# Kernel optimization log

Hardware: AMD Instinct MI355X
Metric: run time of the kernel (lower is better)

The kernel has to match this reference:

```python
import jax, jax.numpy as jnp
import numpy as np

P, N, C, F = 3, 50000, 5, 68   # planes, nodes/plane, classes, in+node feats
E = 150000                     # edges/plane
EF, NF = 64, 64                # edge_features, node_features

def setup_inputs() -> dict:
    key = jax.random.key(0)
    ks = jax.random.split(key, 10)
    s = 0.1
    return {
        "x": jax.random.normal(ks[0], (P, N, C, F), jnp.float32),
        "edge_index": jax.random.randint(ks[1], (P, 2, E), 0, N, jnp.int64),
        "ew1": s * jax.random.normal(ks[2], (P, C, 2 * F, EF), jnp.float32),
        "eb1": s * jax.random.normal(ks[3], (P, C, EF), jnp.float32),
        "ew2": s * jax.random.normal(ks[4], (P, C, EF, 1), jnp.float32),
        "eb2": s * jax.random.normal(ks[5], (P, C, 1), jnp.float32),
        "nw1": s * jax.random.normal(ks[6], (P, C, 2 * F, NF), jnp.float32),
        "nb1": s * jax.random.normal(ks[7], (P, C, NF), jnp.float32),
        "nw2": s * jax.random.normal(ks[8], (P, C, NF, NF), jnp.float32),
        "nb2": s * jax.random.normal(ks[9], (P, C, NF), jnp.float32),
    }

def _plane(x, ei, ew1, eb1, ew2, eb2, nw1, nb1, nw2, nb2):
    # x: [N, C, F]; ei: [2, E]
    src, dst = ei[0], ei[1]
    x_j = x[src]                                   # [E, C, F] (source)
    x_i = x[dst]                                   # [E, C, F] (target)
    # edge net input is detached in the original module
    e_in = jax.lax.stop_gradient(jnp.concatenate([x_i, x_j], axis=-1))  # [E, C, 2F]
    h = jnp.tanh(jnp.einsum('ecf,cfo->eco', e_in, ew1) + eb1)           # [E, C, EF]
    logit = jnp.einsum('ecf,cfo->eco', h, ew2) + eb2                    # [E, C, 1]
    w = jax.nn.softmax(logit, axis=1)              # softmax over classes
    msg = w * x_j                                  # [E, C, F]
    aggr = jax.ops.segment_sum(msg, dst, num_segments=x.shape[0])       # [N, C, F]
    u_in = jnp.concatenate([x, aggr], axis=-1)     # [N, C, 2F]
    h2 = jnp.tanh(jnp.einsum('ncf,cfo->nco', u_in, nw1) + nb1)          # [N, C, NF]
    return jnp.tanh(jnp.einsum('ncf,cfo->nco', h2, nw2) + nb2)          # [N, C, NF]

def reference(x, edge_index, ew1, eb1, ew2, eb2, nw1, nb1, nw2, nb2):
    return jax.vmap(_plane)(x, edge_index, ew1, eb1, ew2, eb2, nw1, nb1, nw2, nb2)
```

## Files before the change

### kernel.cpp

```cpp
#include <hip/hip_runtime.h>
#include <hip/hip_fp16.h>
#include <math.h>

typedef unsigned int uint;
typedef __fp16 half2_t __attribute__((ext_vector_type(2)));
typedef _Float16 v8h __attribute__((ext_vector_type(8)));
typedef _Float16 v4h __attribute__((ext_vector_type(4)));
typedef float f32v4 __attribute__((ext_vector_type(4)));

#define NUM_P 3
#define NUM_N 50000
#define NUM_C 5
#define NUM_E 150000
#define CF 340
#define NB32 1563
#define TE 128
#define EB2 1172
#define TN 128
#define NB128 391
#define SROW 129
#define NSB 196
#define NSBP 50176

#define AH_T   ((size_t)NUM_P * NUM_N * 170)
#define NW1_T  (NUM_P * NUM_C * 68 * 64)
#define NW2_T  (NUM_P * NUM_C * 32 * 64)
#define LG_T   ((size_t)NUM_P * NUM_C * NUM_E)
#define EWB_T  (NUM_P * NUM_C * 2 * 4 * 640)

__device__ __forceinline__ float fast_tanh(float x) {
    float a = __expf(2.0f * x);
    float t = __builtin_amdgcn_rcpf(a + 1.0f);
    return fmaf(-2.0f, t, 1.0f);
}

__device__ __forceinline__ float dot2f(half2_t a, half2_t b, float c) {
#if __has_builtin(__builtin_amdgcn_fdot2)
    return __builtin_amdgcn_fdot2(a, b, c, false);
#else
    return fmaf((float)a[0], (float)b[0], fmaf((float)a[1], (float)b[1], c));
#endif
}

__device__ __forceinline__ half2_t bc(uint u) { return __builtin_bit_cast(half2_t, u); }

__device__ __forceinline__ uint pk2(float a, float b) {
    half2_t h = __builtin_amdgcn_cvt_pkrtz(a, b);
    return __builtin_bit_cast(uint, h);
}

__device__ __forceinline__ v8h mk8(uint a, uint b, uint c, uint d) {
    uint4 u; u.x = a; u.y = b; u.z = c; u.w = d;
    return __builtin_bit_cast(v8h, u);
}

__global__ __launch_bounds__(256) void convert_x_kernel(
    const float4* __restrict__ x4, uint* __restrict__ xh,
    uint* __restrict__ xn, int write_xn)
{
    __shared__ uint lds[32 * 170];
    const int nb = blockIdx.x % NB32;
    const int p  = blockIdx.x / NB32;
    const int n0 = nb * 32;
    const int nvalid = (n0 + 32 <= NUM_N) ? 32 : (NUM_N - n0);
    const int t = threadIdx.x;

    const float4* src = x4 + ((size_t)p * NUM_N + n0) * 85;
    const int nf4 = nvalid * 85;
    #pragma unroll
    for (int it = 0; it < 11; ++it) {
        const int i = t + it * 256;
        if (i < nf4) {
            const float4 v = src[i];
            lds[2 * i]     = pk2(v.x, v.y);
            lds[2 * i + 1] = pk2(v.z, v.w);
        }
    }
    __syncthreads();

    const int nq = nvalid * 34;
    #pragma unroll 1
    for (int c = 0; c < NUM_C; ++c) {
        uint* dst = xh + ((size_t)(p * NUM_C + c) * NUM_N + n0) * 34;
        #pragma unroll
        for (int it = 0; it < 5; ++it) {
            const int i = t + it * 256;
            if (i < nq) {
                const int nl = i / 34, j = i - nl * 34;
                dst[i] = lds[nl * 170 + c * 34 + j];
            }
        }
    }

    if (write_xn) {
        uint* dstn = xn + ((size_t)p * NUM_N + n0) * 170;
        const int tot = nvalid * 170;
        #pragma unroll
        for (int it = 0; it < 22; ++it) {
            const int i = t + it * 256;
            if (i < tot) dstn[i] = lds[i];
        }
    }
}

__global__ __launch_bounds__(256) void pack_pairs_kernel(
    const float* __restrict__ in, uint* __restrict__ outp, int total)
{
    int i = blockIdx.x * 256 + threadIdx.x;
    if (i >= total) return;
    int t = i >> 6, o = i & 63;
    outp[i] = pk2(in[t * 128 + o], in[t * 128 + 64 + o]);
}

__global__ __launch_bounds__(256) void pack_edge_mfma_kernel(
    const float* __restrict__ ew1, uint* __restrict__ ewb)
{
    int i = blockIdx.x * 256 + threadIdx.x;
    if (i >= EWB_T) return;
    int g    = i / 5120;
    int rem  = i - g * 5120;
    int s    = rem / 2560;
    int rem2 = rem - s * 2560;
    int nt   = rem2 / 640;
    int u    = rem2 - nt * 640;

    int f0, o; bool valid;
    if (u < 512) {
        int kt = u >> 8, uu = u & 255;
        int lane = uu >> 2, pp = uu & 3;
        f0 = kt * 32 + (lane >> 4) * 8 + 2 * pp;
        o  = nt * 16 + (lane & 15);
        valid = true;
    } else {
        int uu = u - 512;
        int lane = uu >> 1, pp = uu & 1;
        f0 = 64 + (lane >> 4) * 4 + 2 * pp;
        o  = nt * 16 + (lane & 15);
        valid = ((lane >> 4) == 0);
    }
    float w0 = 0.f, w1 = 0.f;
    if (valid) {
        int f = s * 68 + f0;
        w0 = ew1[((size_t)g * 136 + f) * 64 + o];
        w1 = ew1[((size_t)g * 136 + f + 1) * 64 + o];
    }
    ewb[i] = pk2(w0, w1);
}

__global__ __launch_bounds__(128) void edge_mfma_kernel(
    const uint*  __restrict__ xh,
    const int*   __restrict__ ei,
    const uint*  __restrict__ ewb,
    const float* __restrict__ eb1,
    const float* __restrict__ ew2,
    const float* __restrict__ eb2,
    float*       __restrict__ logits)
{
    __shared__ uint smem[TE * 40];
    __shared__ int  ids[2][TE];

    const int g    = blockIdx.x / EB2;
    const int blk  = blockIdx.x - g * EB2;
    const int p    = g / NUM_C;
    const int e0   = blk * TE;
    const int t    = threadIdx.x;
    const int lane = t & 63;
    const int wv   = t >> 6;
    const int col  = lane & 15;
    const int G    = lane >> 4;

    {
        const int e  = e0 + t;
        const int ec = (e < NUM_E) ? e : (NUM_E - 1);
        ids[0][t] = ei[(p * 2 + 0) * NUM_E + ec];
        ids[1][t] = ei[(p * 2 + 1) * NUM_E + ec];
    }
    {
        const uint2 z = make_uint2(0u, 0u);
        *(uint2*)&smem[t * 40 + 34] = z;
        *(uint2*)&smem[t * 40 + 36] = z;
        *(uint2*)&smem[t * 40 + 38] = z;
    }

    const uint* slice = xh + (size_t)g * NUM_N * 34;

    float b1v[4], w2v[4];
    #pragma unroll
    for (int nt = 0; nt < 4; ++nt) {
        b1v[nt] = eb1[g * 64 + nt * 16 + col];
        w2v[nt] = ew2[g * 64 + nt * 16 + col];
    }

    f32v4 acc[4][4];
    #pragma unroll
    for (int m = 0; m < 4; ++m)
        #pragma unroll
        for (int nt = 0; nt < 4; ++nt) {
            f32v4 a = {b1v[nt], b1v[nt], b1v[nt], b1v[nt]};
            acc[m][nt] = a;
        }
    __syncthreads();

    #pragma unroll 1
    for (int side = 0; side < 2; ++side) {
        const int* idr = ids[1 - side];
        #pragma unroll
        for (int k = 0; k < 17; ++k) {
            const int i2 = t + TE * k;
            const int e  = i2 / 17, j2 = i2 - e * 17;
            const uint2 v = *(const uint2*)(slice + (size_t)idr[e] * 34 + 2 * j2);
            *(uint2*)&smem[e * 40 + 2 * j2] = v;
        }
        __syncthreads();

        const uint* wb = ewb + (size_t)((g * 2 + side) * 4) * 640;
        v8h B0[4], B1[4]; v4h B2[4];
        #pragma unroll
        for (int nt = 0; nt < 4; ++nt) {
            const uint* fb = wb + nt * 640;
            B0[nt] = __builtin_bit_cast(v8h, *(const uint4*)(fb + lane * 4));
            B1[nt] = __builtin_bit_cast(v8h, *(const uint4*)(fb + 256 + lane * 4));
            B2[nt] = __builtin_bit_cast(v4h, *(const uint2*)(fb + 512 + lane * 2));
        }

        #pragma unroll
        for (int m = 0; m < 4; ++m) {
            const uint* rp = &smem[(wv * 64 + m * 16 + col) * 40];
            const v8h A0 = __builtin_bit_cast(v8h, *(const uint4*)(rp + G * 4));
            const v8h A1 = __builtin_bit_cast(v8h, *(const uint4*)(rp + 16 + G * 4));
            const v4h A2 = __builtin_bit_cast(v4h, *(const uint2*)(rp + 32 + G * 2));
            #pragma unroll
            for (int nt = 0; nt < 4; ++nt) {
                acc[m][nt] = __builtin_amdgcn_mfma_f32_16x16x32_f16(A0, B0[nt], acc[m][nt], 0, 0, 0);
                acc[m][nt] = __builtin_amdgcn_mfma_f32_16x16x32_f16(A1, B1[nt], acc[m][nt], 0, 0, 0);
                acc[m][nt] = __builtin_amdgcn_mfma_f32_16x16x16f16(A2, B2[nt], acc[m][nt], 0, 0, 0);
            }
        }
        __syncthreads();
    }

    float* elds = (float*)smem;
    #pragma unroll
    for (int m = 0; m < 4; ++m) {
        #pragma unroll
        for (int r = 0; r < 4; ++r) {
            float part = 0.f;
            #pragma unroll
            for (int nt = 0; nt < 4; ++nt)
                part = fmaf(w2v[nt], fast_tanh(acc[m][nt][r]), part);
            elds[(wv * 64 + m * 16 + G * 4 + r) * 20 + col] = part;
        }
    }
    const float4 s0 = *(const float4*)&elds[t * 20 + 0];
    const float4 s1 = *(const float4*)&elds[t * 20 + 4];
    const float4 s2 = *(const float4*)&elds[t * 20 + 8];
    const float4 s3 = *(const float4*)&elds[t * 20 + 12];
    float lg = ((s0.x + s0.y) + (s0.z + s0.w)) + ((s1.x + s1.y) + (s1.z + s1.w))
             + ((s2.x + s2.y) + (s2.z + s2.w)) + ((s3.x + s3.y) + (s3.z + s3.w))
             + eb2[g];
    if (e0 + t < NUM_E) logits[(size_t)g * NUM_E + e0 + t] = lg;
}

__global__ __launch_bounds__(256) void deg_kernel(
    const int* __restrict__ ei, int* __restrict__ deg)
{
    const int i = blockIdx.x * 256 + threadIdx.x;
    if (i >= NUM_P * NUM_E) return;
    const int p = i / NUM_E, e = i - p * NUM_E;
    const int dst = ei[(p * 2 + 1) * NUM_E + e];
    atomicAdd(&deg[p * NUM_N + dst], 1);
}

__global__ __launch_bounds__(256) void scan_block_kernel(
    const int* __restrict__ deg, int* __restrict__ intra, int* __restrict__ bsum)
{
    __shared__ int s[256];
    const int blk = blockIdx.x % NSB;
    const int p   = blockIdx.x / NSB;
    const int t   = threadIdx.x;
    const int n   = blk * 256 + t;
    const int d   = (n < NUM_N) ? deg[p * NUM_N + n] : 0;
    s[t] = d;
    __syncthreads();
    #pragma unroll
    for (int o = 1; o < 256; o <<= 1) {
        int v = (t >= o) ? s[t - o] : 0;
        __syncthreads();
        s[t] += v;
        __syncthreads();
    }
    if (n < NUM_N) intra[p * NSBP + n] = s[t] - d;
    if (t == 255) bsum[p * NSB + blk] = s[255];
}

__global__ __launch_bounds__(256) void scan_seg_kernel(
    const int* __restrict__ bsum, int* __restrict__ segoff)
{
    __shared__ int s[256];
    const int t = threadIdx.x;
    #pragma unroll 1
    for (int p = 0; p < NUM_P; ++p) {
        const int b = (t < NSB) ? bsum[p * NSB + t] : 0;
        s[t] = b;
        __syncthreads();
        #pragma unroll
        for (int o = 1; o < 256; o <<= 1) {
            int v = (t >= o) ? s[t - o] : 0;
            __syncthreads();
            s[t] += v;
            __syncthreads();
        }
        if (t < NSB) segoff[p * NSB + t] = s[t] - b;
        __syncthreads();
    }
}

__global__ __launch_bounds__(256) void fill_kernel(
    const int* __restrict__ ei, int* __restrict__ cursor,
    const int* __restrict__ intra, const int* __restrict__ segoff,
    int* __restrict__ csr_src, int* __restrict__ csr_eid)
{
    const int i = blockIdx.x * 256 + threadIdx.x;
    if (i >= NUM_P * NUM_E) return;
    const int p = i / NUM_E, e = i - p * NUM_E;
    const int src = ei[(p * 2 + 0) * NUM_E + e];
    const int dst = ei[(p * 2 + 1) * NUM_E + e];
    const int slot = atomicAdd(&cursor[p * NUM_N + dst], 1);
    const int pos  = segoff[p * NSB + (dst >> 8)] + intra[p * NSBP + dst] + slot;
    csr_src[(size_t)p * NUM_E + pos] = src;
    csr_eid[(size_t)p * NUM_E + pos] = e;
}

__global__ __launch_bounds__(256) void gather_kernel(
    const uint*  __restrict__ xn,
    const float* __restrict__ logits,
    const int*   __restrict__ csr_src,
    const int*   __restrict__ csr_eid,
    const int*   __restrict__ deg,
    const int*   __restrict__ intra,
    const int*   __restrict__ segoff,
    uint*        __restrict__ aggr)
{
    const int wslot = threadIdx.x >> 6;
    const int lane  = threadIdx.x & 63;
    const int gw = blockIdx.x * 4 + wslot;
    const int p  = gw / NUM_N;
    const int n  = gw - p * NUM_N;

    const int dg   = deg[p * NUM_N + n];
    const int off0 = segoff[p * NSB + (n >> 8)] + intra[p * NSBP + n];

    const int q1 = lane + 64, q2 = lane + 128;
    const int c0 = lane / 34;
    const int c1 = q1 / 34;
    const int c2 = q2 / 34;

    float a0 = 0.f, a1 = 0.f, a2 = 0.f, a3 = 0.f, a4 = 0.f, a5 = 0.f;

    #pragma unroll 1
    for (int d = 0; d < dg; ++d) {
        const int src = csr_src[(size_t)p * NUM_E + off0 + d];
        const int e   = csr_eid[(size_t)p * NUM_E + off0 + d];

        float l[NUM_C];
        #pragma unroll
        for (int c = 0; c < NUM_C; ++c)
            l[c] = logits[(size_t)(p * NUM_C + c) * NUM_E + e];
        float m = l[0];
        #pragma unroll
        for (int c = 1; c < NUM_C; ++c) m = fmaxf(m, l[c]);
        float s = 0.f;
        #pragma unroll
        for (int c = 0; c < NUM_C; ++c) { l[c] = __expf(l[c] - m); s += l[c]; }
        const float inv = __builtin_amdgcn_rcpf(s);
        const float wt0 = l[0] * inv, wt1 = l[1] * inv, wt2 = l[2] * inv,
                    wt3 = l[3] * inv, wt4 = l[4] * inv;

        const float wa = (c0 == 0) ? wt0 : wt1;
        const float wb = (c1 == 1) ? wt1 : (c1 == 2) ? wt2 : wt3;
        const float wc = (c2 == 3) ? wt3 : wt4;

        const uint* row = xn + (size_t)(p * NUM_N + src) * 170;
        const uint u0 = row[lane];
        const uint u1 = row[q1];
        const uint u2 = (lane < 42) ? row[q2] : 0u;
        const half2_t h0 = bc(u0), h1 = bc(u1), h2 = bc(u2);
        a0 = fmaf(wa, (float)h0[0], a0);
        a1 = fmaf(wa, (float)h0[1], a1);
        a2 = fmaf(wb, (float)h1[0], a2);
        a3 = fmaf(wb, (float)h1[1], a3);
        a4 = fmaf(wc, (float)h2[0], a4);
        a5 = fmaf(wc, (float)h2[1], a5);
    }

    const int i0 = lane - c0 * 34;
    const int i1 = q1 - c1 * 34;
    const int i2 = q2 - c2 * 34;
    aggr[((size_t)(p * NUM_C + c0) * NUM_N + n) * 34 + i0] = pk2(a0, a1);
    aggr[((size_t)(p * NUM_C + c1) * NUM_N + n) * 34 + i1] = pk2(a2, a3);
    if (lane < 42)
        aggr[((size_t)(p * NUM_C + c2) * NUM_N + n) * 34 + i2] = pk2(a4, a5);
}

__global__ __launch_bounds__(256) void edge_scatter_kernel(
    const uint*  __restrict__ xh,
    const int*   __restrict__ ei,
    const float* __restrict__ logits,
    uint*        __restrict__ aggr)
{
    const int wslot = threadIdx.x >> 6;
    const int lane  = threadIdx.x & 63;
    const int gw    = blockIdx.x * 4 + wslot;
    const int p     = gw / NUM_E;
    const int e     = gw - p * NUM_E;

    const int src = ei[(p * 2 + 0) * NUM_E + e];
    const int dst = ei[(p * 2 + 1) * NUM_E + e];

    float l[NUM_C];
    #pragma unroll
    for (int c = 0; c < NUM_C; ++c)
        l[c] = logits[(size_t)(p * NUM_C + c) * NUM_E + e];
    float m = l[0];
    #pragma unroll
    for (int c = 1; c < NUM_C; ++c) m = fmaxf(m, l[c]);
    float s = 0.f;
    #pragma unroll
    for (int c = 0; c < NUM_C; ++c) { l[c] = __expf(l[c] - m); s += l[c]; }
    const float inv = __builtin_amdgcn_rcpf(s);
    const float wt0 = l[0] * inv, wt1 = l[1] * inv, wt2 = l[2] * inv,
                wt3 = l[3] * inv, wt4 = l[4] * inv;

    #pragma unroll
    for (int k = 0; k < 3; ++k) {
        const int q = lane + 64 * k;
        if (q < 170) {
            const int c   = q / 34;
            const int idx = q - c * 34;
            const float wv = (c == 0) ? wt0 : (c == 1) ? wt1 : (c == 2) ? wt2
                           : (c == 3) ? wt3 : wt4;
            const uint xv = xh[((size_t)(p * NUM_C + c) * NUM_N + src) * 34 + idx];
            half2_t mv = __builtin_amdgcn_cvt_pkrtz(wv, wv) * bc(xv);
            uint* ap = aggr + ((size_t)(p * NUM_C + c) * NUM_N + dst) * 34 + idx;
            unsafeAtomicAdd((__half2*)ap, __builtin_bit_cast(__half2, mv));
        }
    }
}

__global__ __launch_bounds__(128) void node_mfma_kernel(
    const uint*  __restrict__ xh,
    const uint*  __restrict__ aggr,
    const uint*  __restrict__ nwp,
    const uint*  __restrict__ n2p,
    const float* __restrict__ nb1,
    const float* __restrict__ nb2,
    float*       __restrict__ out)
{
    __shared__ uint smem[TN * 40];

    const int g    = blockIdx.x / NB128;
    const int blk  = blockIdx.x - g * NB128;
    const int p    = g / NUM_C;
    const int c    = g - p * NUM_C;
    const int n0   = blk * TN;
    const int t    = threadIdx.x;
    const int lane = t & 63;
    const int wv   = t >> 6;
    const int col  = lane & 15;
    const int G    = lane >> 4;
    const int nvalid = (n0 + TN <= NUM_N) ? TN : (NUM_N - n0);
    const int lim2   = nvalid * 17;

    {
        const uint2 z = make_uint2(0u, 0u);
        *(uint2*)&smem[t * 40 + 34] = z;
        *(uint2*)&smem[t * 40 + 36] = z;
        *(uint2*)&smem[t * 40 + 38] = z;
    }

    const uint* wgp = nwp + (size_t)g * 68 * 64;

    float b1v[4];
    #pragma unroll
    for (int nt = 0; nt < 4; ++nt) b1v[nt] = nb1[g * 64 + nt * 16 + col];

    f32v4 acc[4][4];
    #pragma unroll
    for (int m = 0; m < 4; ++m)
        #pragma unroll
        for (int nt = 0; nt < 4; ++nt) {
            f32v4 a = {b1v[nt], b1v[nt], b1v[nt], b1v[nt]};
            acc[m][nt] = a;
        }

    #pragma unroll 1
    for (int side = 0; side < 2; ++side) {
        const uint* srcp = (side == 0 ? xh : aggr) + ((size_t)g * NUM_N + n0) * 34;
        #pragma unroll
        for (int k = 0; k < 17; ++k) {
            const int i2  = t + TN * k;
            const int i2c = (i2 < lim2) ? i2 : (lim2 - 1);
            const uint2 v = *(const uint2*)(srcp + 2 * i2c);
            const int nl = i2 / 17, j2 = i2 - nl * 17;
            *(uint2*)&smem[nl * 40 + 2 * j2] = v;
        }
        __syncthreads();

        v8h B0[4], B1[4]; v4h B2[4];
        #pragma unroll
        for (int nt = 0; nt < 4; ++nt) {
            const int oc = nt * 16 + col;
            const int r0 = side * 34 + G * 4;
            B0[nt] = mk8(wgp[(r0 + 0) * 64 + oc], wgp[(r0 + 1) * 64 + oc],
                         wgp[(r0 + 2) * 64 + oc], wgp[(r0 + 3) * 64 + oc]);
            const int r1 = r0 + 16;
            B1[nt] = mk8(wgp[(r1 + 0) * 64 + oc], wgp[(r1 + 1) * 64 + oc],
                         wgp[(r1 + 2) * 64 + oc], wgp[(r1 + 3) * 64 + oc]);
            uint b2a = (G == 0) ? wgp[(side * 34 + 32) * 64 + oc] : 0u;
            uint b2b = (G == 0) ? wgp[(side * 34 + 33) * 64 + oc] : 0u;
            uint2 u2; u2.x = b2a; u2.y = b2b;
            B2[nt] = __builtin_bit_cast(v4h, u2);
        }

        #pragma unroll
        for (int m = 0; m < 4; ++m) {
            const uint* rp = &smem[(wv * 64 + m * 16 + col) * 40];
            const v8h A0 = __builtin_bit_cast(v8h, *(const uint4*)(rp + G * 4));
            const v8h A1 = __builtin_bit_cast(v8h, *(const uint4*)(rp + 16 + G * 4));
            const v4h A2 = __builtin_bit_cast(v4h, *(const uint2*)(rp + 32 + G * 2));
            #pragma unroll
            for (int nt = 0; nt < 4; ++nt) {
                acc[m][nt] = __builtin_amdgcn_mfma_f32_16x16x32_f16(A0, B0[nt], acc[m][nt], 0, 0, 0);
                acc[m][nt] = __builtin_amdgcn_mfma_f32_16x16x32_f16(A1, B1[nt], acc[m][nt], 0, 0, 0);
                acc[m][nt] = __builtin_amdgcn_mfma_f32_16x16x16f16(A2, B2[nt], acc[m][nt], 0, 0, 0);
            }
        }
        __syncthreads();
    }

    _Float16* hl = (_Float16*)smem;
    #pragma unroll
    for (int m = 0; m < 4; ++m)
        #pragma unroll
        for (int nt = 0; nt < 4; ++nt)
            #pragma unroll
            for (int r = 0; r < 4; ++r)
                hl[(wv * 64 + m * 16 + G * 4 + r) * 72 + nt * 16 + col] =
                    (_Float16)fast_tanh(acc[m][nt][r]);

    const uint* w2p = n2p + (size_t)g * 32 * 64;
    float b2v[4];
    #pragma unroll
    for (int nt = 0; nt < 4; ++nt) b2v[nt] = nb2[g * 64 + nt * 16 + col];

    f32v4 acc2[4][4];
    #pragma unroll
    for (int m = 0; m < 4; ++m)
        #pragma unroll
        for (int nt = 0; nt < 4; ++nt) {
            f32v4 a = {b2v[nt], b2v[nt], b2v[nt], b2v[nt]};
            acc2[m][nt] = a;
        }

    v8h C0[4], C1[4];
    #pragma unroll
    for (int nt = 0; nt < 4; ++nt) {
        const int oc = nt * 16 + col;
        C0[nt] = mk8(w2p[(G * 4 + 0) * 64 + oc], w2p[(G * 4 + 1) * 64 + oc],
                     w2p[(G * 4 + 2) * 64 + oc], w2p[(G * 4 + 3) * 64 + oc]);
        C1[nt] = mk8(w2p[(16 + G * 4 + 0) * 64 + oc], w2p[(16 + G * 4 + 1) * 64 + oc],
                     w2p[(16 + G * 4 + 2) * 64 + oc], w2p[(16 + G * 4 + 3) * 64 + oc]);
    }

    #pragma unroll
    for (int m = 0; m < 4; ++m) {
        const uint* rp = &smem[(wv * 64 + m * 16 + col) * 36];
        const v8h A0 = __builtin_bit_cast(v8h, *(const uint4*)(rp + G * 4));
        const v8h A1 = __builtin_bit_cast(v8h, *(const uint4*)(rp + 16 + G * 4));
        #pragma unroll
        for (int nt = 0; nt < 4; ++nt) {
            acc2[m][nt] = __builtin_amdgcn_mfma_f32_16x16x32_f16(A0, C0[nt], acc2[m][nt], 0, 0, 0);
            acc2[m][nt] = __builtin_amdgcn_mfma_f32_16x16x32_f16(A1, C1[nt], acc2[m][nt], 0, 0, 0);
        }
    }
    __syncthreads();

    float* elds = (float*)smem;
    #pragma unroll
    for (int pass = 0; pass < 2; ++pass) {
        #pragma unroll
        for (int m = 0; m < 4; ++m)
            #pragma unroll
            for (int r = 0; r < 4; ++r) {
                const int row = wv * 64 + m * 16 + G * 4 + r;
                elds[row * 40 + col]      = fast_tanh(acc2[m][2 * pass][r]);
                elds[row * 40 + 16 + col] = fast_tanh(acc2[m][2 * pass + 1][r]);
            }
        if (t < nvalid) {
            float* op = out + ((size_t)(p * NUM_N + n0 + t) * NUM_C + c) * 64 + pass * 32;
            #pragma unroll
            for (int q = 0; q < 8; ++q)
                *(float4*)(op + q * 4) = *(const float4*)&elds[t * 40 + q * 4];
        }
    }
}

__device__ __forceinline__ void dot_side(const uint* __restrict__ xp,
                                         const uint* __restrict__ wp,
                                         float acc[64])
{
    uint2 cur = *(const uint2*)(xp);
    #pragma unroll 1
    for (int j = 0; j < 17; ++j) {
        const int jn = (j < 16) ? (j + 1) : 16;
        const uint2 nxt = *(const uint2*)(xp + jn * 2);
        const half2_t a0 = bc(cur.x);
        const half2_t a1 = bc(cur.y);
        const uint* w0 = wp + (2 * j) * 64;
        #pragma unroll
        for (int o = 0; o < 64; ++o)
            acc[o] = dot2f(a0, bc(w0[o]), acc[o]);
        const uint* w1 = w0 + 64;
        #pragma unroll
        for (int o = 0; o < 64; ++o)
            acc[o] = dot2f(a1, bc(w1[o]), acc[o]);
        cur = nxt;
    }
}

__global__ __launch_bounds__(128) void node_kernel(
    const float* __restrict__ x,
    const uint*  __restrict__ aggr,
    const uint*  __restrict__ nwp,
    const uint*  __restrict__ n2p,
    const float* __restrict__ nb1,
    const float* __restrict__ nb2,
    float*       __restrict__ out)
{
    __shared__ uint buf[34][SROW];

    const int g   = blockIdx.x / NB128;
    const int blk = blockIdx.x - g * NB128;
    const int p   = g / NUM_C;
    const int c   = g - p * NUM_C;
    const int n0  = blk * TN;
    const int t   = threadIdx.x;
    const int nvalid = (n0 + TN <= NUM_N) ? TN : (NUM_N - n0);
    const int lim2 = nvalid * 17;

    float acc[64];
    const float* b1 = nb1 + g * 64;
    #pragma unroll
    for (int o4 = 0; o4 < 64; o4 += 4) {
        const float4 bv = *(const float4*)(b1 + o4);
        acc[o4] = bv.x; acc[o4 + 1] = bv.y; acc[o4 + 2] = bv.z; acc[o4 + 3] = bv.w;
    }
    const uint* wg = nwp + (size_t)g * 68 * 64;

    #pragma unroll
    for (int k = 0; k < 34; ++k) {
        const int i  = t + TN * k;
        const int nl = i / 34, j = i - nl * 34;
        const int nn = (nl < nvalid) ? (n0 + nl) : n0;
        const float2 v = *(const float2*)(x + ((size_t)p * NUM_N + nn) * CF
                                          + c * 68 + 2 * j);
        buf[j][nl] = pk2(v.x, v.y);
    }
    __syncthreads();
    #pragma unroll 1
    for (int j = 0; j < 34; ++j) {
        const half2_t a = bc(buf[j][t]);
        const uint* w = wg + j * 64;
        #pragma unroll
        for (int o = 0; o < 64; ++o) acc[o] = dot2f(a, bc(w[o]), acc[o]);
    }
    __syncthreads();

    {
        const uint* srcp = aggr + ((size_t)g * NUM_N + n0) * 34;
        #pragma unroll
        for (int k = 0; k < 17; ++k) {
            const int i2  = t + TN * k;
            const int i2c = (i2 < lim2) ? i2 : (lim2 - 1);
            const uint2 v = *(const uint2*)(srcp + 2 * i2c);
            const int nl = i2 / 17, j2 = i2 - nl * 17;
            buf[2 * j2][nl]     = v.x;
            buf[2 * j2 + 1][nl] = v.y;
        }
    }
    __syncthreads();
    #pragma unroll 1
    for (int j = 0; j < 34; ++j) {
        const half2_t a = bc(buf[j][t]);
        const uint* w = wg + (34 + j) * 64;
        #pragma unroll
        for (int o = 0; o < 64; ++o) acc[o] = dot2f(a, bc(w[o]), acc[o]);
    }

    uint h2p[32];
    #pragma unroll
    for (int f2 = 0; f2 < 32; ++f2)
        h2p[f2] = pk2(fast_tanh(acc[2 * f2]), fast_tanh(acc[2 * f2 + 1]));

    const float* b2 = nb2 + g * 64;
    float acc2[64];
    #pragma unroll
    for (int o4 = 0; o4 < 64; o4 += 4) {
        const float4 bv = *(const float4*)(b2 + o4);
        acc2[o4] = bv.x; acc2[o4 + 1] = bv.y; acc2[o4 + 2] = bv.z; acc2[o4 + 3] = bv.w;
    }
    const uint* w2g = n2p + (size_t)g * 32 * 64;
    #pragma unroll
    for (int f2 = 0; f2 < 32; ++f2) {
        const half2_t hv = bc(h2p[f2]);
        const uint* wr = w2g + f2 * 64;
        #pragma unroll
        for (int o = 0; o < 64; ++o)
            acc2[o] = dot2f(hv, bc(wr[o]), acc2[o]);
    }

    if (t < nvalid) {
        float* op = out + ((size_t)(p * NUM_N + n0 + t) * NUM_C + c) * 64;
        #pragma unroll
        for (int o4 = 0; o4 < 64; o4 += 4) {
            float4 ov;
            ov.x = fast_tanh(acc2[o4 + 0]);
            ov.y = fast_tanh(acc2[o4 + 1]);
            ov.z = fast_tanh(acc2[o4 + 2]);
            ov.w = fast_tanh(acc2[o4 + 3]);
            *(float4*)(op + o4) = ov;
        }
    }
}

extern "C" void kernel_launch(void* const* d_in, const int* in_sizes, int n_in,
                              void* d_out, int out_size, void* d_ws, size_t ws_size,
                              hipStream_t stream)
{
    (void)in_sizes; (void)n_in; (void)out_size;

    const float* x   = (const float*)d_in[0];
    const int*   ei  = (const int*)  d_in[1];
    const float* ew1 = (const float*)d_in[2];
    const float* eb1 = (const float*)d_in[3];
    const float* ew2 = (const float*)d_in[4];
    const float* eb2 = (const float*)d_in[5];
    const float* nw1 = (const float*)d_in[6];
    const float* nb1 = (const float*)d_in[7];
    const float* nw2 = (const float*)d_in[8];
    const float* nb2 = (const float*)d_in[9];
    float*       out = (float*)d_out;

    uint* ws     = (uint*)d_ws;
    uint* aggr_h = ws;
    uint* nwp    = ws + AH_T;
    uint* n2p    = nwp + NW1_T;
    const size_t o_xh = AH_T + NW1_T + NW2_T;
    const bool fits = ws_size >= (o_xh + AH_T) * sizeof(uint);
    uint*  xh     = fits ? (ws + o_xh) : (uint*)d_out;
    uint*  xn     = (uint*)d_out;
    float* logits = (float*)((uint*)d_out + AH_T);
    uint*  ewb    = (uint*)d_out + AH_T + LG_T;

    int* ibase   = (int*)(ewb + EWB_T);
    int* deg     = ibase;
    int* cursor  = ibase + NUM_P * NUM_N;
    int* intra   = cursor + NUM_P * NUM_N;
    int* bsum    = intra + NUM_P * NSBP;
    int* segoff  = bsum + NUM_P * NSB;
    int* csr_src = segoff + NUM_P * NSB;
    int* csr_eid = csr_src + NUM_P * NUM_E;

    convert_x_kernel<<<NUM_P * NB32, 256, 0, stream>>>(
        (const float4*)x, xh, xn, fits ? 1 : 0);
    pack_edge_mfma_kernel<<<(EWB_T + 255) / 256, 256, 0, stream>>>(ew1, ewb);
    pack_pairs_kernel<<<(NW1_T + 255) / 256, 256, 0, stream>>>(nw1, nwp, NW1_T);
    pack_pairs_kernel<<<(NW2_T + 255) / 256, 256, 0, stream>>>(nw2, n2p, NW2_T);

    edge_mfma_kernel<<<NUM_P * NUM_C * EB2, 128, 0, stream>>>(
        xh, ei, ewb, eb1, ew2, eb2, logits);

    if (fits) {
        (void)hipMemsetAsync(ibase, 0, (size_t)2 * NUM_P * NUM_N * sizeof(int), stream);
        const int egrid = (NUM_P * NUM_E + 255) / 256;
        deg_kernel<<<egrid, 256, 0, stream>>>(ei, deg);
        scan_block_kernel<<<NUM_P * NSB, 256, 0, stream>>>(deg, intra, bsum);
        scan_seg_kernel<<<1, 256, 0, stream>>>(bsum, segoff);
        fill_kernel<<<egrid, 256, 0, stream>>>(ei, cursor, intra, segoff,
                                               csr_src, csr_eid);
        gather_kernel<<<(NUM_P * NUM_N) / 4, 256, 0, stream>>>(
            xn, logits, csr_src, csr_eid, deg, intra, segoff, aggr_h);
        node_mfma_kernel<<<NUM_P * NUM_C * NB128, 128, 0, stream>>>(
            xh, aggr_h, nwp, n2p, nb1, nb2, out);
    } else {
        (void)hipMemsetAsync(aggr_h, 0, AH_T * sizeof(uint), stream);
        edge_scatter_kernel<<<(NUM_P * NUM_E) / 4, 256, 0, stream>>>(
            xh, ei, logits, aggr_h);
        node_kernel<<<NUM_P * NUM_C * NB128, 128, 0, stream>>>(
            x, aggr_h, nwp, n2p, nb1, nb2, out);
    }
}
```

Measured before the change: 638.1 us.

## Precompute edge softmax weights and split node MFMA tile across four waves

Adds a softmax kernel that turns the per-edge class logits into normalized weights once, so the gather loop loads one precomputed weight per lane instead of recomputing a five-way softmax for every incoming edge. The node MFMA kernel now runs 256 threads per block, with each wave handling 32 rows instead of 64. This halves the accumulator registers per wave and adds a barrier between output passes. The cost is an extra kernel launch, an extra weight buffer in the workspace, and more scattered weight loads in the gather, while the node kernel should gain occupancy.

```diff
diff --git a/kernel.cpp b/kernel.cpp
--- a/kernel.cpp
+++ b/kernel.cpp
@@ -21,6 +21,7 @@
 #define SROW 129
 #define NSB 196
 #define NSBP 50176
+#define NST 44
 
 #define AH_T   ((size_t)NUM_P * NUM_N * 170)
 #define NW1_T  (NUM_P * NUM_C * 68 * 64)
@@ -261,6 +262,27 @@
     if (e0 + t < NUM_E) logits[(size_t)g * NUM_E + e0 + t] = lg;
 }
 
+__global__ __launch_bounds__(256) void softmax_kernel(
+    const float* __restrict__ logits, float* __restrict__ wbuf)
+{
+    const int i = blockIdx.x * 256 + threadIdx.x;
+    if (i >= NUM_P * NUM_E) return;
+    const int p = i / NUM_E, e = i - p * NUM_E;
+    const size_t base = (size_t)p * NUM_C * NUM_E + e;
+    float l[NUM_C];
+    #pragma unroll
+    for (int c = 0; c < NUM_C; ++c) l[c] = logits[base + (size_t)c * NUM_E];
+    float m = l[0];
+    #pragma unroll
+    for (int c = 1; c < NUM_C; ++c) m = fmaxf(m, l[c]);
+    float s = 0.f;
+    #pragma unroll
+    for (int c = 0; c < NUM_C; ++c) { l[c] = __expf(l[c] - m); s += l[c]; }
+    const float inv = __builtin_amdgcn_rcpf(s);
+    #pragma unroll
+    for (int c = 0; c < NUM_C; ++c) wbuf[base + (size_t)c * NUM_E] = l[c] * inv;
+}
+
 __global__ __launch_bounds__(256) void deg_kernel(
     const int* __restrict__ ei, int* __restrict__ deg)
 {
@@ -333,7 +355,7 @@
 
 __global__ __launch_bounds__(256) void gather_kernel(
     const uint*  __restrict__ xn,
-    const float* __restrict__ logits,
+    const float* __restrict__ wbuf,
     const int*   __restrict__ csr_src,
     const int*   __restrict__ csr_eid,
     const int*   __restrict__ deg,
@@ -362,23 +384,9 @@
         const int src = csr_src[(size_t)p * NUM_E + off0 + d];
         const int e   = csr_eid[(size_t)p * NUM_E + off0 + d];
 
-        float l[NUM_C];
-        #pragma unroll
-        for (int c = 0; c < NUM_C; ++c)
-            l[c] = logits[(size_t)(p * NUM_C + c) * NUM_E + e];
-        float m = l[0];
-        #pragma unroll
-        for (int c = 1; c < NUM_C; ++c) m = fmaxf(m, l[c]);
-        float s = 0.f;
-        #pragma unroll
-        for (int c = 0; c < NUM_C; ++c) { l[c] = __expf(l[c] - m); s += l[c]; }
-        const float inv = __builtin_amdgcn_rcpf(s);
-        const float wt0 = l[0] * inv, wt1 = l[1] * inv, wt2 = l[2] * inv,
-                    wt3 = l[3] * inv, wt4 = l[4] * inv;
-
-        const float wa = (c0 == 0) ? wt0 : wt1;
-        const float wb = (c1 == 1) ? wt1 : (c1 == 2) ? wt2 : wt3;
-        const float wc = (c2 == 3) ? wt3 : wt4;
+        const float wa = wbuf[(size_t)(p * NUM_C + c0) * NUM_E + e];
+        const float wb = wbuf[(size_t)(p * NUM_C + c1) * NUM_E + e];
+        const float wc = (lane < 42) ? wbuf[(size_t)(p * NUM_C + c2) * NUM_E + e] : 0.f;
 
         const uint* row = xn + (size_t)(p * NUM_N + src) * 170;
         const uint u0 = row[lane];
@@ -447,7 +455,7 @@
     }
 }
 
-__global__ __launch_bounds__(128) void node_mfma_kernel(
+__global__ __launch_bounds__(256) void node_mfma_kernel(
     const uint*  __restrict__ xh,
     const uint*  __restrict__ aggr,
     const uint*  __restrict__ nwp,
@@ -456,7 +464,7 @@
     const float* __restrict__ nb2,
     float*       __restrict__ out)
 {
-    __shared__ uint smem[TN * 40];
+    __shared__ uint smem[TN * NST];
 
     const int g    = blockIdx.x / NB128;
     const int blk  = blockIdx.x - g * NB128;
@@ -471,11 +479,11 @@
     const int nvalid = (n0 + TN <= NUM_N) ? TN : (NUM_N - n0);
     const int lim2   = nvalid * 17;
 
-    {
+    if (t < TN) {
         const uint2 z = make_uint2(0u, 0u);
-        *(uint2*)&smem[t * 40 + 34] = z;
-        *(uint2*)&smem[t * 40 + 36] = z;
-        *(uint2*)&smem[t * 40 + 38] = z;
+        *(uint2*)&smem[t * NST + 34] = z;
+        *(uint2*)&smem[t * NST + 36] = z;
+        *(uint2*)&smem[t * NST + 38] = z;
     }
 
     const uint* wgp = nwp + (size_t)g * 68 * 64;
@@ -484,25 +492,27 @@
     #pragma unroll
     for (int nt = 0; nt < 4; ++nt) b1v[nt] = nb1[g * 64 + nt * 16 + col];
 
-    f32v4 acc[4][4];
-    #pragma unroll
-    for (int m = 0; m < 4; ++m)
+    f32v4 acc[2][4];
+    #pragma unroll
+    for (int mt = 0; mt < 2; ++mt)
         #pragma unroll
         for (int nt = 0; nt < 4; ++nt) {
             f32v4 a = {b1v[nt], b1v[nt], b1v[nt], b1v[nt]};
-            acc[m][nt] = a;
+            acc[mt][nt] = a;
         }
 
     #pragma unroll 1
     for (int side = 0; side < 2; ++side) {
         const uint* srcp = (side == 0 ? xh : aggr) + ((size_t)g * NUM_N + n0) * 34;
         #pragma unroll
-        for (int k = 0; k < 17; ++k) {
-            const int i2  = t + TN * k;
-            const int i2c = (i2 < lim2) ? i2 : (lim2 - 1);
-            const uint2 v = *(const uint2*)(srcp + 2 * i2c);
-            const int nl = i2 / 17, j2 = i2 - nl * 17;
-            *(uint2*)&smem[nl * 40 + 2 * j2] = v;
+        for (int k = 0; k < 9; ++k) {
+            const int i2 = t + 256 * k;
+            if (i2 < TN * 17) {
+                const int i2c = (i2 < lim2) ? i2 : (lim2 - 1);
+                const uint2 v = *(const uint2*)(srcp + 2 * i2c);
+                const int nl = i2 / 17, j2 = i2 - nl * 17;
+                *(uint2*)&smem[nl * NST + 2 * j2] = v;
+            }
         }
         __syncthreads();
 
@@ -523,16 +533,16 @@
         }
 
         #pragma unroll
-        for (int m = 0; m < 4; ++m) {
-            const uint* rp = &smem[(wv * 64 + m * 16 + col) * 40];
+        for (int mt = 0; mt < 2; ++mt) {
+            const uint* rp = &smem[(wv * 32 + mt * 16 + col) * NST];
             const v8h A0 = __builtin_bit_cast(v8h, *(const uint4*)(rp + G * 4));
             const v8h A1 = __builtin_bit_cast(v8h, *(const uint4*)(rp + 16 + G * 4));
             const v4h A2 = __builtin_bit_cast(v4h, *(const uint2*)(rp + 32 + G * 2));
             #pragma unroll
             for (int nt = 0; nt < 4; ++nt) {
-                acc[m][nt] = __builtin_amdgcn_mfma_f32_16x16x32_f16(A0, B0[nt], acc[m][nt], 0, 0, 0);
-                acc[m][nt] = __builtin_amdgcn_mfma_f32_16x16x32_f16(A1, B1[nt], acc[m][nt], 0, 0, 0);
-                acc[m][nt] = __builtin_amdgcn_mfma_f32_16x16x16f16(A2, B2[nt], acc[m][nt], 0, 0, 0);
+                acc[mt][nt] = __builtin_amdgcn_mfma_f32_16x16x32_f16(A0, B0[nt], acc[mt][nt], 0, 0, 0);
+                acc[mt][nt] = __builtin_amdgcn_mfma_f32_16x16x32_f16(A1, B1[nt], acc[mt][nt], 0, 0, 0);
+                acc[mt][nt] = __builtin_amdgcn_mfma_f32_16x16x16f16(A2, B2[nt], acc[mt][nt], 0, 0, 0);
             }
         }
         __syncthreads();
@@ -540,26 +550,26 @@
 
     _Float16* hl = (_Float16*)smem;
     #pragma unroll
-    for (int m = 0; m < 4; ++m)
+    for (int mt = 0; mt < 2; ++mt)
         #pragma unroll
         for (int nt = 0; nt < 4; ++nt)
             #pragma unroll
             for (int r = 0; r < 4; ++r)
-                hl[(wv * 64 + m * 16 + G * 4 + r) * 72 + nt * 16 + col] =
-                    (_Float16)fast_tanh(acc[m][nt][r]);
+                hl[(wv * 32 + mt * 16 + G * 4 + r) * 72 + nt * 16 + col] =
+                    (_Float16)fast_tanh(acc[mt][nt][r]);
 
     const uint* w2p = n2p + (size_t)g * 32 * 64;
     float b2v[4];
     #pragma unroll
     for (int nt = 0; nt < 4; ++nt) b2v[nt] = nb2[g * 64 + nt * 16 + col];
 
-    f32v4 acc2[4][4];
-    #pragma unroll
-    for (int m = 0; m < 4; ++m)
+    f32v4 acc2[2][4];
+    #pragma unroll
+    for (int mt = 0; mt < 2; ++mt)
         #pragma unroll
         for (int nt = 0; nt < 4; ++nt) {
             f32v4 a = {b2v[nt], b2v[nt], b2v[nt], b2v[nt]};
-            acc2[m][nt] = a;
+            acc2[mt][nt] = a;
         }
 
     v8h C0[4], C1[4];
@@ -573,14 +583,14 @@
     }
 
     #pragma unroll
-    for (int m = 0; m < 4; ++m) {
-        const uint* rp = &smem[(wv * 64 + m * 16 + col) * 36];
+    for (int mt = 0; mt < 2; ++mt) {
+        const uint* rp = &smem[(wv * 32 + mt * 16 + col) * 36];
         const v8h A0 = __builtin_bit_cast(v8h, *(const uint4*)(rp + G * 4));
         const v8h A1 = __builtin_bit_cast(v8h, *(const uint4*)(rp + 16 + G * 4));
         #pragma unroll
         for (int nt = 0; nt < 4; ++nt) {
-            acc2[m][nt] = __builtin_amdgcn_mfma_f32_16x16x32_f16(A0, C0[nt], acc2[m][nt], 0, 0, 0);
-            acc2[m][nt] = __builtin_amdgcn_mfma_f32_16x16x32_f16(A1, C1[nt], acc2[m][nt], 0, 0, 0);
+            acc2[mt][nt] = __builtin_amdgcn_mfma_f32_16x16x32_f16(A0, C0[nt], acc2[mt][nt], 0, 0, 0);
+            acc2[mt][nt] = __builtin_amdgcn_mfma_f32_16x16x32_f16(A1, C1[nt], acc2[mt][nt], 0, 0, 0);
         }
     }
     __syncthreads();
@@ -589,19 +599,23 @@
     #pragma unroll
     for (int pass = 0; pass < 2; ++pass) {
         #pragma unroll
-        for (int m = 0; m < 4; ++m)
+        for (int mt = 0; mt < 2; ++mt)
             #pragma unroll
             for (int r = 0; r < 4; ++r) {
-                const int row = wv * 64 + m * 16 + G * 4 + r;
-                elds[row * 40 + col]      = fast_tanh(acc2[m][2 * pass][r]);
-                elds[row * 40 + 16 + col] = fast_tanh(acc2[m][2 * pass + 1][r]);
+                const int row = wv * 32 + mt * 16 + G * 4 + r;
+                elds[row * NST + col]      = fast_tanh(acc2[mt][2 * pass][r]);
+                elds[row * NST + 16 + col] = fast_tanh(acc2[mt][2 * pass + 1][r]);
             }
-        if (t < nvalid) {
-            float* op = out + ((size_t)(p * NUM_N + n0 + t) * NUM_C + c) * 64 + pass * 32;
+        const int row = wv * 32 + (lane >> 1);
+        if (row < nvalid) {
+            float* op = out + ((size_t)(p * NUM_N + n0 + row) * NUM_C + c) * 64
+                      + pass * 32 + (lane & 1) * 16;
+            const float* ep = &elds[row * NST + (lane & 1) * 16];
             #pragma unroll
-            for (int q = 0; q < 8; ++q)
-                *(float4*)(op + q * 4) = *(const float4*)&elds[t * 40 + q * 4];
-        }
+            for (int q = 0; q < 4; ++q)
+                *(float4*)(op + q * 4) = *(const float4*)(ep + q * 4);
+        }
+        if (pass == 0) __syncthreads();
     }
 }
 
@@ -770,6 +784,7 @@
     int* segoff  = bsum + NUM_P * NSB;
     int* csr_src = segoff + NUM_P * NSB;
     int* csr_eid = csr_src + NUM_P * NUM_E;
+    float* wbuf  = (float*)(csr_eid + NUM_P * NUM_E);
 
     convert_x_kernel<<<NUM_P * NB32, 256, 0, stream>>>(
         (const float4*)x, xh, xn, fits ? 1 : 0);
@@ -783,14 +798,15 @@
     if (fits) {
         (void)hipMemsetAsync(ibase, 0, (size_t)2 * NUM_P * NUM_N * sizeof(int), stream);
         const int egrid = (NUM_P * NUM_E + 255) / 256;
+        softmax_kernel<<<egrid, 256, 0, stream>>>(logits, wbuf);
         deg_kernel<<<egrid, 256, 0, stream>>>(ei, deg);
         scan_block_kernel<<<NUM_P * NSB, 256, 0, stream>>>(deg, intra, bsum);
         scan_seg_kernel<<<1, 256, 0, stream>>>(bsum, segoff);
         fill_kernel<<<egrid, 256, 0, stream>>>(ei, cursor, intra, segoff,
                                                csr_src, csr_eid);
         gather_kernel<<<(NUM_P * NUM_N) / 4, 256, 0, stream>>>(
-            xn, logits, csr_src, csr_eid, deg, intra, segoff, aggr_h);
-        node_mfma_kernel<<<NUM_P * NUM_C * NB128, 128, 0, stream>>>(
+            xn, wbuf, csr_src, csr_eid, deg, intra, segoff, aggr_h);
+        node_mfma_kernel<<<NUM_P * NUM_C * NB128, 256, 0, stream>>>(
             xh, aggr_h, nwp, n2p, nb1, nb2, out);
     } else {
         (void)hipMemsetAsync(aggr_h, 0, AH_T * sizeof(uint), stream);
```

Result: faster. 599.5 us (-6.0%).
